# Kernel optimization log

Hardware: AMD Instinct MI355X
Metric: run time of the kernel (lower is better)

The kernel has to match this reference:

```python
import jax, jax.numpy as jnp
import numpy as np

B, T, D, HS = 4, 4096, 1024, 64

def setup_inputs() -> dict:
    key = jax.random.key(0)
    kx, kq, kk, kv = jax.random.split(key, 4)
    s = 1.0 / np.sqrt(D)  # torch Linear default-ish init scale
    return {
        "x": jax.random.normal(kx, (B, T, D), dtype=jnp.float32),
        "Wq": jax.random.uniform(kq, (D, HS), jnp.float32, -s, s),
        "Wk": jax.random.uniform(kk, (D, HS), jnp.float32, -s, s),
        "Wv": jax.random.uniform(kv, (D, HS), jnp.float32, -s, s),
    }

def reference(x, Wq, Wk, Wv):
    # x: [B,T,D]; Wq/Wk/Wv: [D,HS]
    q = jnp.einsum('btd,dh->bth', x, Wq)
    k = jnp.einsum('btd,dh->bth', x, Wk)
    v = jnp.einsum('btd,dh->bth', x, Wv)
    # NOTE: source scales by C**-0.5 with C = d_model (input dim), not head_size
    scale = jnp.asarray(D, x.dtype) ** -0.5
    weights = jnp.einsum('bqh,bkh->bqk', q, k) * scale  # [B,T,T]
    weights = jax.nn.softmax(weights, axis=-1)
    out = jnp.einsum('bqk,bkh->bqh', weights, v)  # [B,T,HS]
    return out
```

## Files before the change

kernel.cpp:

```cpp
#include <hip/hip_runtime.h>


typedef __bf16 bf16;
typedef __bf16 bf16x4 __attribute__((ext_vector_type(4)));
typedef __bf16 bf16x8 __attribute__((ext_vector_type(8)));
typedef float  f32x16 __attribute__((ext_vector_type(16)));

#define MFMA(a, b, c) __builtin_amdgcn_mfma_f32_32x32x16_bf16(a, b, c, 0, 0, 0)

constexpr int T = 4096, D = 1024, HS = 64;
constexpr int ROWS = 4 * T;
constexpr float QSCL = 0.045084220027797f;

__device__ __forceinline__ void gld16(const void* g, void* l) {
    __builtin_amdgcn_global_load_lds(
        (const __attribute__((address_space(1))) unsigned int*)g,
        (__attribute__((address_space(3))) unsigned int*)l, 16, 0, 0);
}

__device__ inline f32x16 zero16() {
    f32x16 z;
#pragma unroll
    for (int i = 0; i < 16; ++i) z[i] = 0.f;
    return z;
}

__global__ __launch_bounds__(256) void prep_wt(
    const float* __restrict__ Wq, const float* __restrict__ Wk,
    const float* __restrict__ Wv, bf16* __restrict__ Wt)
{
    __shared__ float Xf[64 * 68];
    const int m = blockIdx.x >> 4, dt = blockIdx.x & 15;
    const float* W = (m == 0) ? Wq : ((m == 1) ? Wk : Wv);
    const int d0 = dt * 64;
#pragma unroll
    for (int j = 0; j < 4; ++j) {
        int i = threadIdx.x + 256 * j;
        int dr = i >> 4, c4 = i & 15;
        float4 v = *(const float4*)(W + (size_t)(d0 + dr) * 64 + c4 * 4);
        *(float4*)&Xf[dr * 68 + c4 * 4] = v;
    }
    __syncthreads();
    const float scl = (m == 0) ? QSCL : 1.0f;
#pragma unroll
    for (int j = 0; j < 4; ++j) {
        int o = threadIdx.x + 256 * j;
        int h = o >> 4, dc = o & 15;
        bf16x4 w;
#pragma unroll
        for (int k = 0; k < 4; ++k) w[k] = (bf16)(Xf[(dc * 4 + k) * 68 + h] * scl);
        *(bf16x4*)(Wt + (size_t)(m * 64 + h) * D + d0 + dc * 4) = w;
    }
}

__global__ __launch_bounds__(256, 3) void qkv_proj(
    const float* __restrict__ x, const bf16* __restrict__ Wt,
    bf16* __restrict__ Qg, bf16* __restrict__ Kgt, bf16* __restrict__ Vgt)
{
    __shared__ __align__(16) float Xs[2][64 * 64];
    __shared__ __align__(16) short Ws[2][64 * 64];
    const int tid = threadIdx.x;
    const int w = tid >> 6, lane = tid & 63, ln5 = lane & 31, hi = lane >> 5;
    const int tt = w & 1, hh = w >> 1;
    const int xcd = blockIdx.x & 7, t3 = blockIdx.x >> 3;
    const int which = t3 % 3, mlocal = t3 / 3;
    const int r0 = (xcd * 32 + mlocal) * 64;
    const int wb = tid & 448;

    auto stage = [&](int kc, int buf) {
#pragma unroll
        for (int k2 = 0; k2 < 4; ++k2) {
            int s = k2 * 256 + tid;
            int r = s >> 4, j = s & 15, u = j ^ (r & 15);
            gld16(x + (size_t)(r0 + r) * D + kc * 64 + u * 4,
                  &Xs[buf][(k2 * 256 + wb) * 4]);
        }
#pragma unroll
        for (int k2 = 0; k2 < 2; ++k2) {
            int s = k2 * 256 + tid;
            int h = s >> 3, j = s & 7, u = j ^ (h & 7);
            gld16(Wt + (size_t)(which * 64 + h) * D + kc * 64 + u * 8,
                  &Ws[buf][(k2 * 256 + wb) * 8]);
        }
    };

    f32x16 acc = zero16();
    const int rx = tt * 32 + ln5;
    const int hq = hh * 32 + ln5;
    const int swz = ln5 & 7;

    stage(0, 0);
    __syncthreads();
    for (int kc = 0; kc < 16; ++kc) {
        const int cur = kc & 1;
        if (kc < 15) stage(kc + 1, cur ^ 1);
        const float* Xb = &Xs[cur][0];
        const short* Wb = &Ws[cur][0];
#pragma unroll
        for (int ks = 0; ks < 4; ++ks) {
            int u0 = ks * 4 + hi * 2;
            float4 a = *(const float4*)&Xb[rx * 64 + ((u0)     ^ (rx & 15)) * 4];
            float4 b = *(const float4*)&Xb[rx * 64 + ((u0 + 1) ^ (rx & 15)) * 4];
            bf16x8 fx;
            fx[0] = (bf16)a.x; fx[1] = (bf16)a.y; fx[2] = (bf16)a.z; fx[3] = (bf16)a.w;
            fx[4] = (bf16)b.x; fx[5] = (bf16)b.y; fx[6] = (bf16)b.z; fx[7] = (bf16)b.w;
            bf16x8 wf = *(const bf16x8*)&Wb[hq * 64 + (((ks * 2 + hi) ^ swz) * 8)];
            if (which < 2) acc = MFMA(wf, fx, acc);
            else           acc = MFMA(fx, wf, acc);
        }
        __syncthreads();
    }

    if (which < 2) {
        int t = r0 + tt * 32 + ln5;
#pragma unroll
        for (int g = 0; g < 4; ++g) {
            int h0 = hh * 32 + 8 * g + 4 * hi;
            bf16x4 v;
#pragma unroll
            for (int k = 0; k < 4; ++k) v[k] = (bf16)acc[4 * g + k];
            if (which == 0) {
                *(bf16x4*)(Qg + (size_t)t * HS + h0) = v;
            } else {
                int j = (h0 >> 3) ^ (t & 7);
                *(bf16x4*)(Kgt + (size_t)t * HS + j * 8 + 4 * hi) = v;
            }
        }
    } else {
        int hr = hh * 32 + ln5;
#pragma unroll
        for (int g = 0; g < 4; ++g) {
            int t0 = tt * 32 + 8 * g + 4 * hi;
            bf16x4 v;
#pragma unroll
            for (int k = 0; k < 4; ++k) v[k] = (bf16)acc[4 * g + k];
            int j = (t0 >> 3) ^ (hr & 7);
            *(bf16x4*)(Vgt + (size_t)r0 * HS + hr * 64 + j * 8 + 4 * hi) = v;
        }
    }
}

__global__ __launch_bounds__(256, 2) void attn(
    const bf16* __restrict__ Qg, const bf16* __restrict__ Kgt,
    const bf16* __restrict__ Vgt, float* __restrict__ Op,
    float* __restrict__ Lp, float* __restrict__ out, int split)
{
    __shared__ __align__(16) short PO[16384];
    __shared__ float Lx[128];

    const int tid = threadIdx.x;
    const int w = tid >> 6, lane = tid & 63, ln5 = lane & 31, hi = lane >> 5;
    const int wq = w & 1, wk = w >> 1;

    int b, qt, half;
    if (split == 4) {
        int rest = blockIdx.x >> 3; qt = rest & 31;
        int combo = (blockIdx.x & 7) + 8 * (rest >> 5);
        b = combo >> 2; half = combo & 3;
    } else if (split == 2) {
        int c2 = blockIdx.x & 7; b = c2 >> 1; half = c2 & 1; qt = blockIdx.x >> 3;
    } else { b = blockIdx.x & 3; half = 0; qt = blockIdx.x >> 2; }

    const int rbase = b * T;
    const int seg = T / split;
    const int kb0 = rbase + half * seg;
    const int nc = seg / 64;
    const int qrow0 = rbase + qt * 128 + wq * 64;

    bf16x8 bq[2][4];
    {
        const bf16* qp = Qg + (size_t)(qrow0 + ln5) * HS + hi * 8;
#pragma unroll
        for (int qs = 0; qs < 2; ++qs)
#pragma unroll
            for (int ks = 0; ks < 4; ++ks)
                bq[qs][ks] = *(const bf16x8*)(qp + (size_t)qs * 32 * HS + ks * 16);
    }

    const bf16* Kc = Kgt + (size_t)kb0 * HS;
    const bf16* Vc = Vgt + (size_t)kb0 * HS;

    f32x16 O00 = zero16(), O01 = zero16(), O10 = zero16(), O11 = zero16();
    float l0 = 0.f, l1 = 0.f;
    short* Pw = &PO[w * 2560];
    const int swz = ln5 & 7;
    const int krow = (wk * 32 + ln5) * 64;
    const int ko0 = krow + ((0 + hi) ^ swz) * 8;
    const int ko1 = krow + ((2 + hi) ^ swz) * 8;
    const int ko2 = krow + ((4 + hi) ^ swz) * 8;
    const int ko3 = krow + ((6 + hi) ^ swz) * 8;
    const int ku0 = ((wk * 4 + 0 + hi) ^ swz) * 8;
    const int ku1 = ((wk * 4 + 2 + hi) ^ swz) * 8;
    const int vr0 = ln5 * 64, vr1 = (32 + ln5) * 64;

    bf16x8 kf0 = *(const bf16x8*)(Kc + ko0);
    bf16x8 kf1 = *(const bf16x8*)(Kc + ko1);
    bf16x8 kf2 = *(const bf16x8*)(Kc + ko2);
    bf16x8 kf3 = *(const bf16x8*)(Kc + ko3);

    for (int c = 0; c < nc; ++c) {
        const bf16* Vb = Vc + (size_t)c * 4096;
        bf16x8 v00 = *(const bf16x8*)(Vb + vr0 + ku0);
        bf16x8 v01 = *(const bf16x8*)(Vb + vr0 + ku1);
        bf16x8 v10 = *(const bf16x8*)(Vb + vr1 + ku0);
        bf16x8 v11 = *(const bf16x8*)(Vb + vr1 + ku1);
        const bool pf = (c + 1 < nc);
        bf16x8 kn0, kn1, kn2, kn3;
        if (pf) {
            const bf16* Kn = Kc + (size_t)(c + 1) * 4096;
            kn0 = *(const bf16x8*)(Kn + ko0);
            kn1 = *(const bf16x8*)(Kn + ko1);
            kn2 = *(const bf16x8*)(Kn + ko2);
            kn3 = *(const bf16x8*)(Kn + ko3);
        }

        f32x16 S0 = zero16(), S1 = zero16();
        S0 = MFMA(kf0, bq[0][0], S0); S1 = MFMA(kf0, bq[1][0], S1);
        S0 = MFMA(kf1, bq[0][1], S0); S1 = MFMA(kf1, bq[1][1], S1);
        S0 = MFMA(kf2, bq[0][2], S0); S1 = MFMA(kf2, bq[1][2], S1);
        S0 = MFMA(kf3, bq[0][3], S0); S1 = MFMA(kf3, bq[1][3], S1);

#pragma unroll
        for (int g = 0; g < 4; ++g) {
            float p0 = __builtin_amdgcn_exp2f(S0[4 * g + 0]);
            float p1 = __builtin_amdgcn_exp2f(S0[4 * g + 1]);
            float p2 = __builtin_amdgcn_exp2f(S0[4 * g + 2]);
            float p3 = __builtin_amdgcn_exp2f(S0[4 * g + 3]);
            l0 += (p0 + p1) + (p2 + p3);
            bf16x4 pv; pv[0] = (bf16)p0; pv[1] = (bf16)p1; pv[2] = (bf16)p2; pv[3] = (bf16)p3;
            *(bf16x4*)&Pw[ln5 * 40 + 8 * g + 4 * hi] = pv;
        }
#pragma unroll
        for (int g = 0; g < 4; ++g) {
            float p0 = __builtin_amdgcn_exp2f(S1[4 * g + 0]);
            float p1 = __builtin_amdgcn_exp2f(S1[4 * g + 1]);
            float p2 = __builtin_amdgcn_exp2f(S1[4 * g + 2]);
            float p3 = __builtin_amdgcn_exp2f(S1[4 * g + 3]);
            l1 += (p0 + p1) + (p2 + p3);
            bf16x4 pv; pv[0] = (bf16)p0; pv[1] = (bf16)p1; pv[2] = (bf16)p2; pv[3] = (bf16)p3;
            *(bf16x4*)&Pw[(32 + ln5) * 40 + 8 * g + 4 * hi] = pv;
        }

        {
            bf16x8 pf0 = *(const bf16x8*)&Pw[ln5 * 40 + hi * 8];
            bf16x8 pf1 = *(const bf16x8*)&Pw[(32 + ln5) * 40 + hi * 8];
            O00 = MFMA(v00, pf0, O00);
            O01 = MFMA(v00, pf1, O01);
            O10 = MFMA(v10, pf0, O10);
            O11 = MFMA(v10, pf1, O11);
            pf0 = *(const bf16x8*)&Pw[ln5 * 40 + 16 + hi * 8];
            pf1 = *(const bf16x8*)&Pw[(32 + ln5) * 40 + 16 + hi * 8];
            O00 = MFMA(v01, pf0, O00);
            O01 = MFMA(v01, pf1, O01);
            O10 = MFMA(v11, pf0, O10);
            O11 = MFMA(v11, pf1, O11);
        }

        if (pf) { kf0 = kn0; kf1 = kn1; kf2 = kn2; kf3 = kn3; }
    }

    l0 += __shfl_xor(l0, 32, 64);
    l1 += __shfl_xor(l1, 32, 64);

    __syncthreads();
    float* Ox = (float*)&PO[0];
    if (wk == 1) {
#pragma unroll
        for (int g = 0; g < 4; ++g)
#pragma unroll
            for (int k = 0; k < 4; ++k) {
                int h0 = 8 * g + 4 * hi + k;
                Ox[wq * 4096 + h0 * 64 + ln5]             = O00[4 * g + k];
                Ox[wq * 4096 + h0 * 64 + 32 + ln5]        = O01[4 * g + k];
                Ox[wq * 4096 + (32 + h0) * 64 + ln5]      = O10[4 * g + k];
                Ox[wq * 4096 + (32 + h0) * 64 + 32 + ln5] = O11[4 * g + k];
            }
        if (hi == 0) { Lx[wq * 64 + ln5] = l0; Lx[wq * 64 + 32 + ln5] = l1; }
    }
    __syncthreads();
    if (wk == 0) {
#pragma unroll
        for (int g = 0; g < 4; ++g)
#pragma unroll
            for (int k = 0; k < 4; ++k) {
                int h0 = 8 * g + 4 * hi + k;
                O00[4 * g + k] += Ox[wq * 4096 + h0 * 64 + ln5];
                O01[4 * g + k] += Ox[wq * 4096 + h0 * 64 + 32 + ln5];
                O10[4 * g + k] += Ox[wq * 4096 + (32 + h0) * 64 + ln5];
                O11[4 * g + k] += Ox[wq * 4096 + (32 + h0) * 64 + 32 + ln5];
            }
        l0 += Lx[wq * 64 + ln5];
        l1 += Lx[wq * 64 + 32 + ln5];

        int q0 = qrow0 + ln5, q1 = qrow0 + 32 + ln5;
        if (split == 1) {
            float i0 = 1.0f / l0, i1 = 1.0f / l1;
#pragma unroll
            for (int g = 0; g < 4; ++g) {
                int h0 = 8 * g + 4 * hi;
                float4 o;
                o.x = O00[4*g+0]*i0; o.y = O00[4*g+1]*i0; o.z = O00[4*g+2]*i0; o.w = O00[4*g+3]*i0;
                *(float4*)(out + (size_t)q0 * HS + h0) = o;
                o.x = O01[4*g+0]*i1; o.y = O01[4*g+1]*i1; o.z = O01[4*g+2]*i1; o.w = O01[4*g+3]*i1;
                *(float4*)(out + (size_t)q1 * HS + h0) = o;
                o.x = O10[4*g+0]*i0; o.y = O10[4*g+1]*i0; o.z = O10[4*g+2]*i0; o.w = O10[4*g+3]*i0;
                *(float4*)(out + (size_t)q0 * HS + 32 + h0) = o;
                o.x = O11[4*g+0]*i1; o.y = O11[4*g+1]*i1; o.z = O11[4*g+2]*i1; o.w = O11[4*g+3]*i1;
                *(float4*)(out + (size_t)q1 * HS + 32 + h0) = o;
            }
        } else {
            float* Od = Op + (size_t)half * ROWS * HS;
#pragma unroll
            for (int g = 0; g < 4; ++g) {
                int h0 = 8 * g + 4 * hi;
                float4 o;
                o.x = O00[4*g+0]; o.y = O00[4*g+1]; o.z = O00[4*g+2]; o.w = O00[4*g+3];
                *(float4*)(Od + (size_t)q0 * HS + h0) = o;
                o.x = O01[4*g+0]; o.y = O01[4*g+1]; o.z = O01[4*g+2]; o.w = O01[4*g+3];
                *(float4*)(Od + (size_t)q1 * HS + h0) = o;
                o.x = O10[4*g+0]; o.y = O10[4*g+1]; o.z = O10[4*g+2]; o.w = O10[4*g+3];
                *(float4*)(Od + (size_t)q0 * HS + 32 + h0) = o;
                o.x = O11[4*g+0]; o.y = O11[4*g+1]; o.z = O11[4*g+2]; o.w = O11[4*g+3];
                *(float4*)(Od + (size_t)q1 * HS + 32 + h0) = o;
            }
            if (hi == 0) {
                Lp[half * ROWS + q0] = l0;
                Lp[half * ROWS + q1] = l1;
            }
        }
    }
}

__global__ __launch_bounds__(256) void attn_reduce(
    const float* __restrict__ Op, const float* __restrict__ Lp,
    float* __restrict__ out, int split)
{
    int idx = blockIdx.x * 256 + threadIdx.x;
    int row = idx >> 4;
    float4 s; s.x = s.y = s.z = s.w = 0.f;
    float lsum = 0.f;
    for (int h = 0; h < split; ++h) {
        float4 a = *(const float4*)(Op + (size_t)h * ROWS * HS + (size_t)idx * 4);
        s.x += a.x; s.y += a.y; s.z += a.z; s.w += a.w;
        lsum += Lp[h * ROWS + row];
    }
    float inv = 1.0f / lsum;
    s.x *= inv; s.y *= inv; s.z *= inv; s.w *= inv;
    *(float4*)(out + (size_t)idx * 4) = s;
}

extern "C" void kernel_launch(void* const* d_in, const int* in_sizes, int n_in,
                              void* d_out, int out_size, void* d_ws, size_t ws_size,
                              hipStream_t stream)
{
    const float* x  = (const float*)d_in[0];
    const float* Wq = (const float*)d_in[1];
    const float* Wk = (const float*)d_in[2];
    const float* Wv = (const float*)d_in[3];
    float* out = (float*)d_out;

    char* ws = (char*)d_ws;
    bf16* Qg  = (bf16*)(ws);
    bf16* Kgt = (bf16*)(ws + ((size_t)2 << 20));
    bf16* Vgt = (bf16*)(ws + ((size_t)4 << 20));
    bf16* Wt  = (bf16*)(ws + ((size_t)6 << 20));
    float* Lp = (float*)(ws + ((size_t)6 << 20));
    float* Op = (float*)(ws + ((size_t)6 << 20) + ((size_t)1 << 19));

    const size_t base = ((size_t)6 << 20) + ((size_t)1 << 19);
    int split = 1;
    if (ws_size >= base + (size_t)4 * ROWS * HS * sizeof(float)) split = 4;
    else if (ws_size >= base + (size_t)2 * ROWS * HS * sizeof(float)) split = 2;

    prep_wt<<<48, 256, 0, stream>>>(Wq, Wk, Wv, Wt);
    qkv_proj<<<768, 256, 0, stream>>>(x, Wt, Qg, Kgt, Vgt);
    attn<<<128 * split, 256, 0, stream>>>(Qg, Kgt, Vgt, Op, Lp, out, split);
    if (split > 1)
        attn_reduce<<<(ROWS * HS / 4) / 256, 256, 0, stream>>>(Op, Lp, out, split);
}
```

Before: 147.8 us.

## Fuse all stages into one cooperative persistent kernel with grid syncs

Replaces the four separate launches (weight prep, QKV projection, split attention, reduction) with one cooperative kernel of 512 blocks that uses grid.sync between stages. The goal is to remove per-launch overhead and the gaps between kernels. In exchange, the projection stage now runs at 2 blocks per CU instead of 3 and uses a grid-stride loop over 768 tiles, which leaves some blocks with an uneven second pass. Grid barriers also add their own cost. If the cooperative launch fails, the code falls back to the original multi-kernel path.

```diff
diff --git a/kernel.cpp b/kernel.cpp
--- a/kernel.cpp
+++ b/kernel.cpp
@@ -1,5 +1,8 @@
 #include <hip/hip_runtime.h>
-
+#include <hip/hip_cooperative_groups.h>
+
+
+namespace cg = cooperative_groups;
 
 typedef __bf16 bf16;
 typedef __bf16 bf16x4 __attribute__((ext_vector_type(4)));
@@ -25,17 +28,17 @@
     return z;
 }
 
-__global__ __launch_bounds__(256) void prep_wt(
-    const float* __restrict__ Wq, const float* __restrict__ Wk,
-    const float* __restrict__ Wv, bf16* __restrict__ Wt)
-{
-    __shared__ float Xf[64 * 68];
-    const int m = blockIdx.x >> 4, dt = blockIdx.x & 15;
+
+__device__ __forceinline__ void prep_body(int item, const float* Wq, const float* Wk,
+        const float* Wv, bf16* Wt, float* Xf )
+{
+    const int tid = threadIdx.x;
+    const int m = item >> 4, dt = item & 15;
     const float* W = (m == 0) ? Wq : ((m == 1) ? Wk : Wv);
     const int d0 = dt * 64;
 #pragma unroll
     for (int j = 0; j < 4; ++j) {
-        int i = threadIdx.x + 256 * j;
+        int i = tid + 256 * j;
         int dr = i >> 4, c4 = i & 15;
         float4 v = *(const float4*)(W + (size_t)(d0 + dr) * 64 + c4 * 4);
         *(float4*)&Xf[dr * 68 + c4 * 4] = v;
@@ -44,7 +47,7 @@
     const float scl = (m == 0) ? QSCL : 1.0f;
 #pragma unroll
     for (int j = 0; j < 4; ++j) {
-        int o = threadIdx.x + 256 * j;
+        int o = tid + 256 * j;
         int h = o >> 4, dc = o & 15;
         bf16x4 w;
 #pragma unroll
@@ -53,16 +56,14 @@
     }
 }
 
-__global__ __launch_bounds__(256, 3) void qkv_proj(
-    const float* __restrict__ x, const bf16* __restrict__ Wt,
-    bf16* __restrict__ Qg, bf16* __restrict__ Kgt, bf16* __restrict__ Vgt)
-{
-    __shared__ __align__(16) float Xs[2][64 * 64];
-    __shared__ __align__(16) short Ws[2][64 * 64];
+__device__ __forceinline__ void proj_body(int it, const float* x, const bf16* Wt,
+        bf16* Qg, bf16* Kgt, bf16* Vgt,
+        float* Xs , short* Ws )
+{
     const int tid = threadIdx.x;
     const int w = tid >> 6, lane = tid & 63, ln5 = lane & 31, hi = lane >> 5;
     const int tt = w & 1, hh = w >> 1;
-    const int xcd = blockIdx.x & 7, t3 = blockIdx.x >> 3;
+    const int xcd = it & 7, t3 = it >> 3;
     const int which = t3 % 3, mlocal = t3 / 3;
     const int r0 = (xcd * 32 + mlocal) * 64;
     const int wb = tid & 448;
@@ -73,14 +74,14 @@
             int s = k2 * 256 + tid;
             int r = s >> 4, j = s & 15, u = j ^ (r & 15);
             gld16(x + (size_t)(r0 + r) * D + kc * 64 + u * 4,
-                  &Xs[buf][(k2 * 256 + wb) * 4]);
+                  &Xs[buf * 4096 + (k2 * 256 + wb) * 4]);
         }
 #pragma unroll
         for (int k2 = 0; k2 < 2; ++k2) {
             int s = k2 * 256 + tid;
             int h = s >> 3, j = s & 7, u = j ^ (h & 7);
             gld16(Wt + (size_t)(which * 64 + h) * D + kc * 64 + u * 8,
-                  &Ws[buf][(k2 * 256 + wb) * 8]);
+                  &Ws[buf * 4096 + (k2 * 256 + wb) * 8]);
         }
     };
 
@@ -94,8 +95,8 @@
     for (int kc = 0; kc < 16; ++kc) {
         const int cur = kc & 1;
         if (kc < 15) stage(kc + 1, cur ^ 1);
-        const float* Xb = &Xs[cur][0];
-        const short* Wb = &Ws[cur][0];
+        const float* Xb = &Xs[cur * 4096];
+        const short* Wb = &Ws[cur * 4096];
 #pragma unroll
         for (int ks = 0; ks < 4; ++ks) {
             int u0 = ks * 4 + hi * 2;
@@ -140,26 +141,22 @@
     }
 }
 
-__global__ __launch_bounds__(256, 2) void attn(
-    const bf16* __restrict__ Qg, const bf16* __restrict__ Kgt,
-    const bf16* __restrict__ Vgt, float* __restrict__ Op,
-    float* __restrict__ Lp, float* __restrict__ out, int split)
-{
-    __shared__ __align__(16) short PO[16384];
-    __shared__ float Lx[128];
-
+__device__ __forceinline__ void attn_body(int bid, int split, const bf16* Qg,
+        const bf16* Kgt, const bf16* Vgt, float* Op, float* Lp, float* out,
+        short* PO , float* Lx )
+{
     const int tid = threadIdx.x;
     const int w = tid >> 6, lane = tid & 63, ln5 = lane & 31, hi = lane >> 5;
     const int wq = w & 1, wk = w >> 1;
 
     int b, qt, half;
     if (split == 4) {
-        int rest = blockIdx.x >> 3; qt = rest & 31;
-        int combo = (blockIdx.x & 7) + 8 * (rest >> 5);
+        int rest = bid >> 3; qt = rest & 31;
+        int combo = (bid & 7) + 8 * (rest >> 5);
         b = combo >> 2; half = combo & 3;
     } else if (split == 2) {
-        int c2 = blockIdx.x & 7; b = c2 >> 1; half = c2 & 1; qt = blockIdx.x >> 3;
-    } else { b = blockIdx.x & 3; half = 0; qt = blockIdx.x >> 2; }
+        int c2 = bid & 7; b = c2 >> 1; half = c2 & 1; qt = bid >> 3;
+    } else { b = bid & 3; half = 0; qt = bid >> 2; }
 
     const int rbase = b * T;
     const int seg = T / split;
@@ -331,11 +328,10 @@
     }
 }
 
-__global__ __launch_bounds__(256) void attn_reduce(
-    const float* __restrict__ Op, const float* __restrict__ Lp,
-    float* __restrict__ out, int split)
-{
-    int idx = blockIdx.x * 256 + threadIdx.x;
+__device__ __forceinline__ void reduce_body(int it, int split,
+        const float* Op, const float* Lp, float* out)
+{
+    int idx = it * 256 + threadIdx.x;
     int row = idx >> 4;
     float4 s; s.x = s.y = s.z = s.w = 0.f;
     float lsum = 0.f;
@@ -349,6 +345,69 @@
     *(float4*)(out + (size_t)idx * 4) = s;
 }
 
+
+__global__ __launch_bounds__(256, 2) void mega(
+    const float* __restrict__ x, const float* __restrict__ Wq,
+    const float* __restrict__ Wk, const float* __restrict__ Wv,
+    bf16* __restrict__ Wt, bf16* __restrict__ Qg, bf16* __restrict__ Kgt,
+    bf16* __restrict__ Vgt, float* __restrict__ Op, float* __restrict__ Lp,
+    float* __restrict__ out)
+{
+    __shared__ __align__(16) char smem[49664];
+    const int bid = blockIdx.x;
+    cg::grid_group grid = cg::this_grid();
+
+    if (bid < 48) prep_body(bid, Wq, Wk, Wv, Wt, (float*)smem);
+    grid.sync();
+
+    for (int it = bid; it < 768; it += 512)
+        proj_body(it, x, Wt, Qg, Kgt, Vgt, (float*)smem, (short*)(smem + 32768));
+    grid.sync();
+
+    attn_body(bid, 4, Qg, Kgt, Vgt, Op, Lp, out,
+              (short*)smem, (float*)(smem + 32768));
+    grid.sync();
+
+    for (int it = bid; it < 1024; it += 512)
+        reduce_body(it, 4, Op, Lp, out);
+}
+
+
+__global__ __launch_bounds__(256) void prep_wt(
+    const float* __restrict__ Wq, const float* __restrict__ Wk,
+    const float* __restrict__ Wv, bf16* __restrict__ Wt)
+{
+    __shared__ float Xf[64 * 68];
+    prep_body(blockIdx.x, Wq, Wk, Wv, Wt, Xf);
+}
+
+__global__ __launch_bounds__(256, 3) void qkv_proj(
+    const float* __restrict__ x, const bf16* __restrict__ Wt,
+    bf16* __restrict__ Qg, bf16* __restrict__ Kgt, bf16* __restrict__ Vgt)
+{
+    __shared__ __align__(16) float Xs[2 * 4096];
+    __shared__ __align__(16) short Ws[2 * 4096];
+    proj_body(blockIdx.x, x, Wt, Qg, Kgt, Vgt, Xs, Ws);
+}
+
+__global__ __launch_bounds__(256, 2) void attn(
+    const bf16* __restrict__ Qg, const bf16* __restrict__ Kgt,
+    const bf16* __restrict__ Vgt, float* __restrict__ Op,
+    float* __restrict__ Lp, float* __restrict__ out, int split)
+{
+    __shared__ __align__(16) short PO[16384];
+    __shared__ float Lx[128];
+    attn_body(blockIdx.x, split, Qg, Kgt, Vgt, Op, Lp, out, PO, Lx);
+}
+
+__global__ __launch_bounds__(256) void attn_reduce(
+    const float* __restrict__ Op, const float* __restrict__ Lp,
+    float* __restrict__ out, int split)
+{
+    reduce_body(blockIdx.x, split, Op, Lp, out);
+}
+
+
 extern "C" void kernel_launch(void* const* d_in, const int* in_sizes, int n_in,
                               void* d_out, int out_size, void* d_ws, size_t ws_size,
                               hipStream_t stream)
@@ -368,8 +427,20 @@
     float* Op = (float*)(ws + ((size_t)6 << 20) + ((size_t)1 << 19));
 
     const size_t base = ((size_t)6 << 20) + ((size_t)1 << 19);
+    const bool can4 = ws_size >= base + (size_t)4 * ROWS * HS * sizeof(float);
+
+    if (can4) {
+        void* kargs[] = {(void*)&x, (void*)&Wq, (void*)&Wk, (void*)&Wv,
+                         (void*)&Wt, (void*)&Qg, (void*)&Kgt, (void*)&Vgt,
+                         (void*)&Op, (void*)&Lp, (void*)&out};
+        hipError_t e = hipLaunchCooperativeKernel((const void*)mega, dim3(512),
+                                                  dim3(256), kargs, 0, stream);
+        if (e == hipSuccess) return;
+        (void)hipGetLastError();
+    }
+
     int split = 1;
-    if (ws_size >= base + (size_t)4 * ROWS * HS * sizeof(float)) split = 4;
+    if (can4) split = 4;
     else if (ws_size >= base + (size_t)2 * ROWS * HS * sizeof(float)) split = 2;
 
     prep_wt<<<48, 256, 0, stream>>>(Wq, Wk, Wv, Wt);
```

Result: slower. 357.2 us (+141.6%).

## Fuse Q, K, V projections into one block per row tile

Applied to the files above, without the earlier changes.

Each block now computes Q, K and V for its 64-row tile with three accumulators, instead of three separate blocks each re-reading the same fp32 x tile. x is loaded through registers, converted to bf16 once, and stored to swizzled LDS while the next tile's weights are fetched asynchronously. This removes two redundant reads of x and the repeated per-use conversion. In exchange the grid shrinks to 256 blocks, LDS use per block grows, and occupancy may drop.

```diff
diff --git a/kernel.cpp b/kernel.cpp
--- a/kernel.cpp
+++ b/kernel.cpp
@@ -53,87 +53,111 @@
     }
 }
 
-__global__ __launch_bounds__(256, 3) void qkv_proj(
+__global__ __launch_bounds__(256) void qkv_proj(
     const float* __restrict__ x, const bf16* __restrict__ Wt,
     bf16* __restrict__ Qg, bf16* __restrict__ Kgt, bf16* __restrict__ Vgt)
 {
-    __shared__ __align__(16) float Xs[2][64 * 64];
-    __shared__ __align__(16) short Ws[2][64 * 64];
+    __shared__ __align__(16) bf16  Xb[2][64 * 64];
+    __shared__ __align__(16) short Ws[2][192 * 64];
     const int tid = threadIdx.x;
     const int w = tid >> 6, lane = tid & 63, ln5 = lane & 31, hi = lane >> 5;
     const int tt = w & 1, hh = w >> 1;
-    const int xcd = blockIdx.x & 7, t3 = blockIdx.x >> 3;
-    const int which = t3 % 3, mlocal = t3 / 3;
+    const int xcd = blockIdx.x & 7, mlocal = blockIdx.x >> 3;
     const int r0 = (xcd * 32 + mlocal) * 64;
     const int wb = tid & 448;
 
-    auto stage = [&](int kc, int buf) {
-#pragma unroll
-        for (int k2 = 0; k2 < 4; ++k2) {
-            int s = k2 * 256 + tid;
-            int r = s >> 4, j = s & 15, u = j ^ (r & 15);
-            gld16(x + (size_t)(r0 + r) * D + kc * 64 + u * 4,
-                  &Xs[buf][(k2 * 256 + wb) * 4]);
-        }
-#pragma unroll
-        for (int k2 = 0; k2 < 2; ++k2) {
+    auto stageW = [&](int kc, int buf) {
+#pragma unroll
+        for (int k2 = 0; k2 < 6; ++k2) {
             int s = k2 * 256 + tid;
             int h = s >> 3, j = s & 7, u = j ^ (h & 7);
-            gld16(Wt + (size_t)(which * 64 + h) * D + kc * 64 + u * 8,
+            gld16(Wt + (size_t)h * D + kc * 64 + u * 8,
                   &Ws[buf][(k2 * 256 + wb) * 8]);
         }
     };
-
-    f32x16 acc = zero16();
+    float4 xra[2], xrb[2];
+    auto stageX_load = [&](int kc) {
+#pragma unroll
+        for (int k = 0; k < 2; ++k) {
+            int e = k * 256 + tid;
+            int r = e >> 3, d0 = (e & 7) * 8;
+            const float* src = x + (size_t)(r0 + r) * D + kc * 64 + d0;
+            xra[k] = *(const float4*)src;
+            xrb[k] = *(const float4*)(src + 4);
+        }
+    };
+    auto stageX_write = [&](int buf) {
+#pragma unroll
+        for (int k = 0; k < 2; ++k) {
+            int e = k * 256 + tid;
+            int r = e >> 3, d0 = (e & 7) * 8;
+            bf16x8 v;
+            v[0] = (bf16)xra[k].x; v[1] = (bf16)xra[k].y;
+            v[2] = (bf16)xra[k].z; v[3] = (bf16)xra[k].w;
+            v[4] = (bf16)xrb[k].x; v[5] = (bf16)xrb[k].y;
+            v[6] = (bf16)xrb[k].z; v[7] = (bf16)xrb[k].w;
+            *(bf16x8*)&Xb[buf][r * 64 + (((d0 >> 3) ^ (r & 7)) * 8)] = v;
+        }
+    };
+
+    f32x16 acc0 = zero16(), acc1 = zero16(), acc2 = zero16();
     const int rx = tt * 32 + ln5;
     const int hq = hh * 32 + ln5;
     const int swz = ln5 & 7;
 
-    stage(0, 0);
+    stageX_load(0); stageW(0, 0); stageX_write(0);
     __syncthreads();
     for (int kc = 0; kc < 16; ++kc) {
         const int cur = kc & 1;
-        if (kc < 15) stage(kc + 1, cur ^ 1);
-        const float* Xb = &Xs[cur][0];
+        if (kc < 15) { stageW(kc + 1, cur ^ 1); stageX_load(kc + 1); }
+        const bf16*  Xc = &Xb[cur][0];
         const short* Wb = &Ws[cur][0];
 #pragma unroll
         for (int ks = 0; ks < 4; ++ks) {
-            int u0 = ks * 4 + hi * 2;
-            float4 a = *(const float4*)&Xb[rx * 64 + ((u0)     ^ (rx & 15)) * 4];
-            float4 b = *(const float4*)&Xb[rx * 64 + ((u0 + 1) ^ (rx & 15)) * 4];
-            bf16x8 fx;
-            fx[0] = (bf16)a.x; fx[1] = (bf16)a.y; fx[2] = (bf16)a.z; fx[3] = (bf16)a.w;
-            fx[4] = (bf16)b.x; fx[5] = (bf16)b.y; fx[6] = (bf16)b.z; fx[7] = (bf16)b.w;
-            bf16x8 wf = *(const bf16x8*)&Wb[hq * 64 + (((ks * 2 + hi) ^ swz) * 8)];
-            if (which < 2) acc = MFMA(wf, fx, acc);
-            else           acc = MFMA(fx, wf, acc);
-        }
+            int g = (ks * 2 + hi) ^ swz;
+            bf16x8 fx = *(const bf16x8*)&Xc[rx * 64 + g * 8];
+            bf16x8 w0 = *(const bf16x8*)&Wb[(hq)       * 64 + g * 8];
+            bf16x8 w1 = *(const bf16x8*)&Wb[(64 + hq)  * 64 + g * 8];
+            bf16x8 w2 = *(const bf16x8*)&Wb[(128 + hq) * 64 + g * 8];
+            acc0 = MFMA(w0, fx, acc0);
+            acc1 = MFMA(w1, fx, acc1);
+            acc2 = MFMA(fx, w2, acc2);
+        }
+        if (kc < 15) stageX_write(cur ^ 1);
         __syncthreads();
     }
 
-    if (which < 2) {
+    {
         int t = r0 + tt * 32 + ln5;
 #pragma unroll
         for (int g = 0; g < 4; ++g) {
             int h0 = hh * 32 + 8 * g + 4 * hi;
             bf16x4 v;
 #pragma unroll
-            for (int k = 0; k < 4; ++k) v[k] = (bf16)acc[4 * g + k];
-            if (which == 0) {
-                *(bf16x4*)(Qg + (size_t)t * HS + h0) = v;
-            } else {
-                int j = (h0 >> 3) ^ (t & 7);
-                *(bf16x4*)(Kgt + (size_t)t * HS + j * 8 + 4 * hi) = v;
-            }
-        }
-    } else {
+            for (int k = 0; k < 4; ++k) v[k] = (bf16)acc0[4 * g + k];
+            *(bf16x4*)(Qg + (size_t)t * HS + h0) = v;
+        }
+    }
+    {
+        int t = r0 + tt * 32 + ln5;
+#pragma unroll
+        for (int g = 0; g < 4; ++g) {
+            int h0 = hh * 32 + 8 * g + 4 * hi;
+            bf16x4 v;
+#pragma unroll
+            for (int k = 0; k < 4; ++k) v[k] = (bf16)acc1[4 * g + k];
+            int j = (h0 >> 3) ^ (t & 7);
+            *(bf16x4*)(Kgt + (size_t)t * HS + j * 8 + 4 * hi) = v;
+        }
+    }
+    {
         int hr = hh * 32 + ln5;
 #pragma unroll
         for (int g = 0; g < 4; ++g) {
             int t0 = tt * 32 + 8 * g + 4 * hi;
             bf16x4 v;
 #pragma unroll
-            for (int k = 0; k < 4; ++k) v[k] = (bf16)acc[4 * g + k];
+            for (int k = 0; k < 4; ++k) v[k] = (bf16)acc2[4 * g + k];
             int j = (t0 >> 3) ^ (hr & 7);
             *(bf16x4*)(Vgt + (size_t)r0 * HS + hr * 64 + j * 8 + 4 * hi) = v;
         }
@@ -373,7 +397,7 @@
     else if (ws_size >= base + (size_t)2 * ROWS * HS * sizeof(float)) split = 2;
 
     prep_wt<<<48, 256, 0, stream>>>(Wq, Wk, Wv, Wt);
-    qkv_proj<<<768, 256, 0, stream>>>(x, Wt, Qg, Kgt, Vgt);
+    qkv_proj<<<256, 256, 0, stream>>>(x, Wt, Qg, Kgt, Vgt);
     attn<<<128 * split, 256, 0, stream>>>(Qg, Kgt, Vgt, Op, Lp, out, split);
     if (split > 1)
         attn_reduce<<<(ROWS * HS / 4) / 256, 256, 0, stream>>>(Op, Lp, out, split);
```

New measurement: 142.9 us. 3.3% less time.
